# Optimization experiments

Hardware: AMD Instinct MI355X
Metric: run time of the kernel (lower is better)

Reference implementation:

```python
import jax, jax.numpy as jnp
import numpy as np

D_ENC = 512
D_DEC = 512
JOINT = 512
VOCAB = 1024


def setup_inputs() -> dict:
    key = jax.random.key(0)
    ks = jax.random.split(key, 7)
    B, T, U = 4, 256, 64
    s_enc = 1.0 / np.sqrt(D_ENC)
    s_dec = 1.0 / np.sqrt(D_DEC)
    s_out = 1.0 / np.sqrt(JOINT)
    return {
        "encoder_out": jax.random.normal(ks[0], (B, T, 1, D_ENC), dtype=jnp.float32),
        "decoder_out": jax.random.normal(ks[1], (B, 1, U, D_DEC), dtype=jnp.float32),
        # torch.nn.Linear stores weight as (out, in); uniform(-1/sqrt(in), 1/sqrt(in))
        "W_enc": jax.random.uniform(ks[2], (JOINT, D_ENC), jnp.float32, -s_enc, s_enc),
        "b_enc": jax.random.uniform(ks[3], (JOINT,), jnp.float32, -s_enc, s_enc),
        "W_dec": jax.random.uniform(ks[4], (JOINT, D_DEC), jnp.float32, -s_dec, s_dec),
        "W_out": jax.random.uniform(ks[5], (VOCAB, JOINT), jnp.float32, -s_out, s_out),
        "b_out": jax.random.uniform(ks[6], (VOCAB,), jnp.float32, -s_out, s_out),
    }


def reference(encoder_out, decoder_out, W_enc, b_enc, W_dec, W_out, b_out):
    # Project each side in its small shape first (B,T,1,J) and (B,1,U,J),
    # then broadcast-add over (T,U), tanh, output GEMM -> (B,T,U,V).
    enc = jnp.einsum("btud,jd->btuj", encoder_out, W_enc) + b_enc  # (B,T,1,J)
    dec = jnp.einsum("btud,jd->btuj", decoder_out, W_dec)          # (B,1,U,J)
    h = jnp.tanh(enc + dec)                                        # (B,T,U,J)
    return jnp.einsum("btuj,vj->btuv", h, W_out) + b_out           # (B,T,U,V)
```

## Files before the change

### kernel.cpp

```cpp
#include <hip/hip_runtime.h>
#include <hip/hip_bf16.h>


typedef __attribute__((ext_vector_type(8))) short short8;
typedef __attribute__((ext_vector_type(4))) float f32x4;

#define SZ0 524288
#define SZ1 131072
#define SZ2 262144
#define SZ3 512
#define SZ4 262144
#define SZ5 524288
#define SZ6 1024
#define CU0 0
#define CU1 524288
#define CU2 655360
#define CU3 917504
#define CU4 918016
#define CU5 1180160
#define CU6 1704448
#define CTOT 1705472

__global__ void detect_kernel(const void* p0, const void* p1, const void* p2,
                              const void* p3, const void* p4, const void* p5,
                              const void* p6, int* flags) {
  const void* ps[7] = {p0, p1, p2, p3, p4, p5, p6};
  const int sz[7] = {SZ0, SZ1, SZ2, SZ3, SZ4, SZ5, SZ6};
  const int w = threadIdx.x >> 6;
  const int l = threadIdx.x & 63;
  if (w >= 7) return;
  const unsigned short* u = (const unsigned short*)ps[w];
  const int lim = sz[w] < 1024 ? sz[w] : 1024;
  int bad = 0;
  for (int j = l; j < lim; j += 64) {
    const unsigned e = (u[j] >> 7) & 0xFFu;
    if (e >= 0x8Eu) bad = 1;
  }
  const unsigned long long b = __ballot(bad);
  if (l == 0) flags[w] = (b != 0ULL) ? 1 : 0;
}

__global__ __launch_bounds__(256) void convert_kernel(
    const void* p0, const void* p1, const void* p2, const void* p3,
    const void* p4, const void* p5, const void* p6,
    const int* __restrict__ flags, __hip_bfloat16* __restrict__ dst) {
  const int gid = blockIdx.x * 256 + threadIdx.x;
  if (gid >= CTOT) return;
  int t, local;
  const void* p;
  if (gid < CU1)      { t = 0; local = gid - CU0; p = p0; }
  else if (gid < CU2) { t = 1; local = gid - CU1; p = p1; }
  else if (gid < CU3) { t = 2; local = gid - CU2; p = p2; }
  else if (gid < CU4) { t = 3; local = gid - CU3; p = p3; }
  else if (gid < CU5) { t = 4; local = gid - CU4; p = p4; }
  else if (gid < CU6) { t = 5; local = gid - CU5; p = p5; }
  else                { t = 6; local = gid - CU6; p = p6; }
  __hip_bfloat16 v;
  if (flags[t])
    v = __float2bfloat16(((const float*)p)[local]);
  else
    v = ((const __hip_bfloat16*)p)[local];
  dst[gid] = v;
}

__device__ __forceinline__ void gemm_bt_body(
    const __hip_bfloat16* __restrict__ A, const __hip_bfloat16* __restrict__ Bw,
    const __hip_bfloat16* __restrict__ bias, float* __restrict__ C,
    int M, int N, int K, int bid,
    __hip_bfloat16* sA, __hip_bfloat16* sB) {
  const int tid = threadIdx.x;
  const int w = tid >> 6;
  const int l = tid & 63;
  const int ntiles = N >> 7;
  const int mt = bid / ntiles;
  const int nt = bid % ntiles;
  const int m0 = mt << 7;
  const int n0 = nt << 7;
  const int wm = (w >> 1) << 6;
  const int wn = (w & 1) << 6;
  const int r16 = l & 15;
  const int q = l >> 4;

  f32x4 acc[4][4] = {};

  const int srow_in = l >> 3;
  const int scol = (l & 7) << 3;

  for (int k0 = 0; k0 < K; k0 += 64) {
#pragma unroll
    for (int i = 0; i < 4; ++i) {
      const int c = (w << 2) + i;
      const int row = (c << 3) + srow_in;
      const __hip_bfloat16* gA = A + (size_t)(m0 + row) * K + k0 + scol;
      const __hip_bfloat16* gB = Bw + (size_t)(n0 + row) * K + k0 + scol;
      __builtin_amdgcn_global_load_lds(
          (const __attribute__((address_space(1))) void*)gA,
          (__attribute__((address_space(3))) void*)(sA + (c << 9) + (l << 3)),
          16, 0, 0);
      __builtin_amdgcn_global_load_lds(
          (const __attribute__((address_space(1))) void*)gB,
          (__attribute__((address_space(3))) void*)(sB + (c << 9) + (l << 3)),
          16, 0, 0);
    }
    __syncthreads();

#pragma unroll
    for (int kk = 0; kk < 2; ++kk) {
      const int kc = (kk << 5) + (q << 3);
      short8 af[4], bf[4];
#pragma unroll
      for (int mi = 0; mi < 4; ++mi)
        af[mi] = *(const short8*)(sA + (wm + (mi << 4) + r16) * 64 + kc);
#pragma unroll
      for (int ni = 0; ni < 4; ++ni)
        bf[ni] = *(const short8*)(sB + (wn + (ni << 4) + r16) * 64 + kc);
#pragma unroll
      for (int mi = 0; mi < 4; ++mi)
#pragma unroll
        for (int ni = 0; ni < 4; ++ni)
          acc[mi][ni] = __builtin_amdgcn_mfma_f32_16x16x32_bf16(
              af[mi], bf[ni], acc[mi][ni], 0, 0, 0);
    }
    __syncthreads();
  }

#pragma unroll
  for (int ni = 0; ni < 4; ++ni) {
    const int col = n0 + wn + (ni << 4) + r16;
    const float bc = bias ? __bfloat162float(bias[col]) : 0.0f;
#pragma unroll
    for (int mi = 0; mi < 4; ++mi) {
      const int rowb = m0 + wm + (mi << 4) + (q << 2);
#pragma unroll
      for (int i = 0; i < 4; ++i)
        C[(size_t)(rowb + i) * N + col] = acc[mi][ni][i] + bc;
    }
  }
}

__global__ __launch_bounds__(256) void proj_kernel(
    const __hip_bfloat16* __restrict__ enc, const __hip_bfloat16* __restrict__ Wenc,
    const __hip_bfloat16* __restrict__ benc,
    const __hip_bfloat16* __restrict__ dec, const __hip_bfloat16* __restrict__ Wdec,
    float* __restrict__ Pe, float* __restrict__ Pd) {
  __shared__ __align__(16) __hip_bfloat16 sA[128 * 64];
  __shared__ __align__(16) __hip_bfloat16 sB[128 * 64];
  if (blockIdx.x < 32)
    gemm_bt_body(enc, Wenc, benc, Pe, 1024, 512, 512, blockIdx.x, sA, sB);
  else
    gemm_bt_body(dec, Wdec, nullptr, Pd, 256, 512, 512, blockIdx.x - 32, sA, sB);
}

__global__ __launch_bounds__(256) void gemm_fused(
    const float* __restrict__ Pe, const float* __restrict__ Pd,
    const __hip_bfloat16* __restrict__ Bw,
    const __hip_bfloat16* __restrict__ bias, float* __restrict__ out) {
  __shared__ __align__(16) __hip_bfloat16 sA[128 * 64];
  __shared__ __align__(16) __hip_bfloat16 sB[128 * 64];
  const int tid = threadIdx.x;
  const int w = tid >> 6;
  const int l = tid & 63;
  const int mt = blockIdx.x >> 3;
  const int nt = blockIdx.x & 7;
  const int m0 = mt << 7;
  const int n0 = nt << 7;
  const int wm = (w >> 1) << 6;
  const int wn = (w & 1) << 6;
  const int r16 = l & 15;
  const int q = l >> 4;
  f32x4 acc[4][4] = {};
  const int arow = tid >> 3;
  const int acol = (tid & 7) << 3;

  for (int k0 = 0; k0 < 512; k0 += 64) {
#pragma unroll
    for (int i = 0; i < 4; ++i) {
      const int c = (w << 2) + i;
      const int row = (c << 3) + (l >> 3);
      const int col = (l & 7) << 3;
      __builtin_amdgcn_global_load_lds(
          (const __attribute__((address_space(1))) void*)(
              Bw + (size_t)(n0 + row) * 512 + k0 + col),
          (__attribute__((address_space(3))) void*)(sB + (c << 9) + (l << 3)),
          16, 0, 0);
    }
#pragma unroll
    for (int c2 = 0; c2 < 4; ++c2) {
      const int row = arow + (c2 << 5);
      const int m = m0 + row;
      const int e = m >> 6;
      const int dd = ((m >> 14) << 6) | (m & 63);
      const float* pe = Pe + (size_t)e * 512 + k0 + acol;
      const float* pd = Pd + (size_t)dd * 512 + k0 + acol;
      const f32x4 e0 = *(const f32x4*)pe, e1 = *(const f32x4*)(pe + 4);
      const f32x4 g0 = *(const f32x4*)pd, g1 = *(const f32x4*)(pd + 4);
      short8 hv;
#pragma unroll
      for (int j = 0; j < 4; ++j) {
        float s = e0[j] + g0[j];
        float t = 1.0f - 2.0f / (__expf(2.0f * s) + 1.0f);
        __hip_bfloat16 hb = __float2bfloat16(t);
        hv[j] = *(const short*)&hb;
        s = e1[j] + g1[j];
        t = 1.0f - 2.0f / (__expf(2.0f * s) + 1.0f);
        hb = __float2bfloat16(t);
        hv[4 + j] = *(const short*)&hb;
      }
      *(short8*)(sA + row * 64 + acol) = hv;
    }
    __syncthreads();
#pragma unroll
    for (int kk = 0; kk < 2; ++kk) {
      const int kc = (kk << 5) + (q << 3);
      short8 af[4], bf[4];
#pragma unroll
      for (int mi = 0; mi < 4; ++mi)
        af[mi] = *(const short8*)(sA + (wm + (mi << 4) + r16) * 64 + kc);
#pragma unroll
      for (int ni = 0; ni < 4; ++ni)
        bf[ni] = *(const short8*)(sB + (wn + (ni << 4) + r16) * 64 + kc);
#pragma unroll
      for (int mi = 0; mi < 4; ++mi)
#pragma unroll
        for (int ni = 0; ni < 4; ++ni)
          acc[mi][ni] = __builtin_amdgcn_mfma_f32_16x16x32_bf16(
              af[mi], bf[ni], acc[mi][ni], 0, 0, 0);
    }
    __syncthreads();
  }

#pragma unroll
  for (int ni = 0; ni < 4; ++ni) {
    const int col = n0 + wn + (ni << 4) + r16;
    const float bc = __bfloat162float(bias[col]);
#pragma unroll
    for (int mi = 0; mi < 4; ++mi) {
      const int rowb = m0 + wm + (mi << 4) + (q << 2);
#pragma unroll
      for (int i = 0; i < 4; ++i)
        out[(size_t)(rowb + i) * 1024 + col] = acc[mi][ni][i] + bc;
    }
  }
}

extern "C" void kernel_launch(void* const* d_in, const int* in_sizes, int n_in,
                              void* d_out, int out_size, void* d_ws,
                              size_t ws_size, hipStream_t stream) {
  char* ws = (char*)d_ws;
  int* flags = (int*)ws;
  __hip_bfloat16* cp = (__hip_bfloat16*)(ws + 256);
  float* Pe = (float*)(ws + (4ull << 20));
  float* Pd = (float*)(ws + (6ull << 20));

  detect_kernel<<<dim3(1), dim3(512), 0, stream>>>(
      d_in[0], d_in[1], d_in[2], d_in[3], d_in[4], d_in[5], d_in[6], flags);
  convert_kernel<<<dim3((CTOT + 255) / 256), dim3(256), 0, stream>>>(
      d_in[0], d_in[1], d_in[2], d_in[3], d_in[4], d_in[5], d_in[6], flags, cp);

  const __hip_bfloat16* enc_c = cp + CU0;
  const __hip_bfloat16* dec_c = cp + CU1;
  const __hip_bfloat16* Wenc_c = cp + CU2;
  const __hip_bfloat16* benc_c = cp + CU3;
  const __hip_bfloat16* Wdec_c = cp + CU4;
  const __hip_bfloat16* Wout_c = cp + CU5;
  const __hip_bfloat16* bout_c = cp + CU6;

  proj_kernel<<<dim3(40), dim3(256), 0, stream>>>(enc_c, Wenc_c, benc_c,
                                                  dec_c, Wdec_c, Pe, Pd);
  gemm_fused<<<dim3(4096), dim3(256), 0, stream>>>(
      Pe, Pd, Wout_c, bout_c, (float*)d_out);
}
```

Measured before the change: 465.4 us.

## Compute full tanh row tile once into LDS and sweep all vocab columns

The joint GEMM kernel now has each 512-thread block compute its 128-row tile of tanh(enc+dec) across the full 512-wide K dimension once, storing it in a swizzled 128KB LDS buffer. It then loops over all vocab columns in 256-wide chunks, double-buffering W_out K-slices through global_load_lds. This removes the 8x redundant tanh recomputation and Pe/Pd reloads of the old per-(m,n)-tile grid and overlaps weight loads with MFMA work. The cost is very large LDS use, which limits occupancy to about one block per CU, and the grid shrinks to 512 blocks.

Measured after the change: 410.2 us. 11.9% less time.

```diff
diff --git a/kernel.cpp b/kernel.cpp
--- a/kernel.cpp
+++ b/kernel.cpp
@@ -151,95 +151,128 @@
     gemm_bt_body(dec, Wdec, nullptr, Pd, 256, 512, 512, blockIdx.x - 32, sA, sB);
 }
 
-__global__ __launch_bounds__(256) void gemm_fused(
+__global__ __launch_bounds__(512, 2) void gemm_joint(
     const float* __restrict__ Pe, const float* __restrict__ Pd,
     const __hip_bfloat16* __restrict__ Bw,
     const __hip_bfloat16* __restrict__ bias, float* __restrict__ out) {
-  __shared__ __align__(16) __hip_bfloat16 sA[128 * 64];
-  __shared__ __align__(16) __hip_bfloat16 sB[128 * 64];
-  const int tid = threadIdx.x;
-  const int w = tid >> 6;
-  const int l = tid & 63;
-  const int mt = blockIdx.x >> 3;
-  const int nt = blockIdx.x & 7;
-  const int m0 = mt << 7;
-  const int n0 = nt << 7;
-  const int wm = (w >> 1) << 6;
-  const int wn = (w & 1) << 6;
+  __shared__ __align__(16) __hip_bfloat16 sH[128 * 512];
+  __shared__ __align__(16) __hip_bfloat16 sB[2][256 * 32];
+
+  const int t = threadIdx.x;
+  const int w = t >> 6;
+  const int l = t & 63;
   const int r16 = l & 15;
   const int q = l >> 4;
+  const int m0 = blockIdx.x << 7;
+
+  auto stage = [&](int iter, int buf) {
+    const int n0 = (iter >> 4) << 8;
+    const int k0 = (iter & 15) << 5;
+#pragma unroll
+    for (int j = 0; j < 2; ++j) {
+      const int chunk = (w << 7) + (j << 6) + l;
+      const int row = chunk >> 2;
+      const int cc = chunk & 3;
+      const __hip_bfloat16* src =
+          Bw + (size_t)(n0 + row) * 512 + k0 + ((cc ^ (row & 3)) << 3);
+      __builtin_amdgcn_global_load_lds(
+          (const __attribute__((address_space(1))) void*)src,
+          (__attribute__((address_space(3))) void*)(&sB[buf][0] + (chunk << 3)),
+          16, 0, 0);
+    }
+  };
+
+  stage(0, 0);
+
+  {
+    const int r = t & 127;
+    const int seg = t >> 7;
+    const int m = m0 + r;
+    const int e = m >> 6;
+    const int d = ((m >> 14) << 6) | (r & 63);
+    const float* pe = Pe + (size_t)e * 512 + (seg << 7);
+    const float* pd = Pd + (size_t)d * 512 + (seg << 7);
+#pragma unroll
+    for (int i = 0; i < 16; ++i) {
+      const int cc = (seg << 4) + i;
+      const f32x4 a0 = *(const f32x4*)(pe + (i << 3));
+      const f32x4 a1 = *(const f32x4*)(pe + (i << 3) + 4);
+      const f32x4 b0 = *(const f32x4*)(pd + (i << 3));
+      const f32x4 b1 = *(const f32x4*)(pd + (i << 3) + 4);
+      short8 hv;
+#pragma unroll
+      for (int jj = 0; jj < 4; ++jj) {
+        float s = a0[jj] + b0[jj];
+        float tv = 1.0f - 2.0f / (__expf(2.0f * s) + 1.0f);
+        __hip_bfloat16 hb = __float2bfloat16(tv);
+        hv[jj] = *(const short*)&hb;
+        s = a1[jj] + b1[jj];
+        tv = 1.0f - 2.0f / (__expf(2.0f * s) + 1.0f);
+        hb = __float2bfloat16(tv);
+        hv[4 + jj] = *(const short*)&hb;
+      }
+      *(short8*)(sH + (r << 9) + ((cc ^ (r & 7)) << 3)) = hv;
+    }
+  }
+  __syncthreads();
+
+  const int wm = (w >> 2) << 6;
+  const int wn = (w & 3) << 6;
   f32x4 acc[4][4] = {};
-  const int arow = tid >> 3;
-  const int acol = (tid & 7) << 3;
-
-  for (int k0 = 0; k0 < 512; k0 += 64) {
-#pragma unroll
-    for (int i = 0; i < 4; ++i) {
-      const int c = (w << 2) + i;
-      const int row = (c << 3) + (l >> 3);
-      const int col = (l & 7) << 3;
-      __builtin_amdgcn_global_load_lds(
-          (const __attribute__((address_space(1))) void*)(
-              Bw + (size_t)(n0 + row) * 512 + k0 + col),
-          (__attribute__((address_space(3))) void*)(sB + (c << 9) + (l << 3)),
-          16, 0, 0);
-    }
-#pragma unroll
-    for (int c2 = 0; c2 < 4; ++c2) {
-      const int row = arow + (c2 << 5);
-      const int m = m0 + row;
-      const int e = m >> 6;
-      const int dd = ((m >> 14) << 6) | (m & 63);
-      const float* pe = Pe + (size_t)e * 512 + k0 + acol;
-      const float* pd = Pd + (size_t)dd * 512 + k0 + acol;
-      const f32x4 e0 = *(const f32x4*)pe, e1 = *(const f32x4*)(pe + 4);
-      const f32x4 g0 = *(const f32x4*)pd, g1 = *(const f32x4*)(pd + 4);
-      short8 hv;
-#pragma unroll
-      for (int j = 0; j < 4; ++j) {
-        float s = e0[j] + g0[j];
-        float t = 1.0f - 2.0f / (__expf(2.0f * s) + 1.0f);
-        __hip_bfloat16 hb = __float2bfloat16(t);
-        hv[j] = *(const short*)&hb;
-        s = e1[j] + g1[j];
-        t = 1.0f - 2.0f / (__expf(2.0f * s) + 1.0f);
-        hb = __float2bfloat16(t);
-        hv[4 + j] = *(const short*)&hb;
+
+  int aoff[4], boff[4];
+#pragma unroll
+  for (int mi = 0; mi < 4; ++mi) aoff[mi] = (wm + (mi << 4) + r16) << 9;
+#pragma unroll
+  for (int ni = 0; ni < 4; ++ni) {
+    const int row = wn + (ni << 4) + r16;
+    boff[ni] = (row << 5) + ((q ^ (row & 3)) << 3);
+  }
+  const int swzA = r16 & 7;
+
+  int buf = 0;
+  for (int iter = 0; iter < 64; ++iter) {
+    if (iter < 63) stage(iter + 1, buf ^ 1);
+
+    const int cbase = (iter & 15) << 2;
+    const int ch = ((cbase + q) ^ swzA) << 3;
+    short8 af[4], bf[4];
+#pragma unroll
+    for (int mi = 0; mi < 4; ++mi)
+      af[mi] = *(const short8*)(sH + aoff[mi] + ch);
+#pragma unroll
+    for (int ni = 0; ni < 4; ++ni)
+      bf[ni] = *(const short8*)(&sB[buf][0] + boff[ni]);
+#pragma unroll
+    for (int mi = 0; mi < 4; ++mi)
+#pragma unroll
+      for (int ni = 0; ni < 4; ++ni)
+        acc[mi][ni] = __builtin_amdgcn_mfma_f32_16x16x32_bf16(
+            af[mi], bf[ni], acc[mi][ni], 0, 0, 0);
+
+    if ((iter & 15) == 15) {
+      const int n0 = (iter >> 4) << 8;
+#pragma unroll
+      for (int ni = 0; ni < 4; ++ni) {
+        const int col = n0 + wn + (ni << 4) + r16;
+        const float bc = __bfloat162float(bias[col]);
+#pragma unroll
+        for (int mi = 0; mi < 4; ++mi) {
+          const int rowb = m0 + wm + (mi << 4) + (q << 2);
+#pragma unroll
+          for (int i = 0; i < 4; ++i)
+            out[(size_t)(rowb + i) * 1024 + col] = acc[mi][ni][i] + bc;
+        }
       }
-      *(short8*)(sA + row * 64 + acol) = hv;
-    }
+#pragma unroll
+      for (int mi = 0; mi < 4; ++mi)
+#pragma unroll
+        for (int ni = 0; ni < 4; ++ni)
+          acc[mi][ni] = (f32x4){0.0f, 0.0f, 0.0f, 0.0f};
+    }
+
     __syncthreads();
-#pragma unroll
-    for (int kk = 0; kk < 2; ++kk) {
-      const int kc = (kk << 5) + (q << 3);
-      short8 af[4], bf[4];
-#pragma unroll
-      for (int mi = 0; mi < 4; ++mi)
-        af[mi] = *(const short8*)(sA + (wm + (mi << 4) + r16) * 64 + kc);
-#pragma unroll
-      for (int ni = 0; ni < 4; ++ni)
-        bf[ni] = *(const short8*)(sB + (wn + (ni << 4) + r16) * 64 + kc);
-#pragma unroll
-      for (int mi = 0; mi < 4; ++mi)
-#pragma unroll
-        for (int ni = 0; ni < 4; ++ni)
-          acc[mi][ni] = __builtin_amdgcn_mfma_f32_16x16x32_bf16(
-              af[mi], bf[ni], acc[mi][ni], 0, 0, 0);
-    }
-    __syncthreads();
-  }
-
-#pragma unroll
-  for (int ni = 0; ni < 4; ++ni) {
-    const int col = n0 + wn + (ni << 4) + r16;
-    const float bc = __bfloat162float(bias[col]);
-#pragma unroll
-    for (int mi = 0; mi < 4; ++mi) {
-      const int rowb = m0 + wm + (mi << 4) + (q << 2);
-#pragma unroll
-      for (int i = 0; i < 4; ++i)
-        out[(size_t)(rowb + i) * 1024 + col] = acc[mi][ni][i] + bc;
-    }
+    buf ^= 1;
   }
 }
 
@@ -267,6 +300,6 @@
 
   proj_kernel<<<dim3(40), dim3(256), 0, stream>>>(enc_c, Wenc_c, benc_c,
                                                   dec_c, Wdec_c, Pe, Pd);
-  gemm_fused<<<dim3(4096), dim3(256), 0, stream>>>(
+  gemm_joint<<<dim3(512), dim3(512), 0, stream>>>(
       Pe, Pd, Wout_c, bout_c, (float*)d_out);
 }
```
